# Optimization experiments

Hardware: AMD Instinct MI355X
Metric: run time of the kernel (lower is better)

Reference implementation:

```python
import jax, jax.numpy as jnp
import numpy as np

B, N, D, C = 256, 5, 2048, 1000   # batch, nodeNum, inputDim, num_classes
H = 1024                          # GCN hidden dim (dim_hid)
PROTO_M = 0.999                   # args.proto_m EMA momentum
EPS = 1e-12


def normalize_adj(a):
    # symmetric normalization D^-1/2 A D^-1/2 of the all-ones adjacency
    d = jnp.sum(a, axis=1)
    dinv = 1.0 / jnp.sqrt(d)
    return a * dinv[:, None] * dinv[None, :]


def setup_inputs() -> dict:
    key = jax.random.key(0)
    ks = jax.random.split(key, 8)
    x = jax.random.normal(ks[0], (B, N, D), jnp.float32)          # region features (post-backbone)
    target = jax.random.randint(ks[1], (B,), 0, C)                # labels
    prototypes = jax.random.normal(ks[2], (C, N, D), jnp.float32)  # prototype memory bank
    adj = normalize_adj(jnp.ones((N, N), jnp.float32))            # adjMatrix_q
    s = 0.02
    W1 = jax.random.normal(ks[3], (D, H), jnp.float32) * s        # GCN layer 1
    W2 = jax.random.normal(ks[4], (H, D), jnp.float32) * s        # GCN layer 2
    Wg = jax.random.normal(ks[5], (N * D, D), jnp.float32) * s    # fc_g
    bg = jnp.zeros((D,), jnp.float32)
    Wc = jax.random.normal(ks[6], (D, C), jnp.float32) * s        # fc_cls
    bc = jnp.zeros((C,), jnp.float32)
    return dict(x=x, target=target, prototypes=prototypes, adj=adj,
                W1=W1, W2=W2, Wg=Wg, bg=bg, Wc=Wc, bc=bc)


def reference(x, target, prototypes, adj, W1, W2, Wg, bg, Wc, bc):
    # --- Res_Gcn (non-proto path): 2-layer GCN over the N region nodes ---
    h = jax.nn.relu(jnp.einsum('nm,bmd,dh->bnh', adj, x, W1))      # [B,N,H]
    nodes = jnp.einsum('nm,bmh,hd->bnd', adj, h, W2)               # [B,N,D]
    g = nodes.reshape(B, N * D) @ Wg + bg                          # fc_g -> [B,D]
    pred = g @ Wc + bc                                             # fc_cls -> [B,C]

    # --- sequential per-sample EMA scatter-update of prototype bank ---
    # order matters for duplicate labels, so use lax.scan (sequential)
    def step(protos, inp):
        feat, label = inp                                          # feat: [N,D]
        new = protos[label] * PROTO_M + (1.0 - PROTO_M) * feat
        return protos.at[label].set(new), None

    protos, _ = jax.lax.scan(step, prototypes, (x, target))

    # F.normalize(prototypes, p=2, dim=1): L2 norm over the node axis
    norm = jnp.sqrt(jnp.sum(protos * protos, axis=1, keepdims=True))
    protos = protos / jnp.maximum(norm, EPS)
    return pred, protos
```

## Files before the change

kernel.cpp:

```cpp
#include <hip/hip_runtime.h>
#include <hip/hip_bf16.h>
#include <math.h>

#define BB 256
#define NN 5
#define DD 2048
#define CC 1000
#define HH 1024
#define PROTO_M 0.999f

typedef unsigned short u16;
typedef __attribute__((ext_vector_type(8))) short short8;
typedef __attribute__((ext_vector_type(4))) float f32x4;

__device__ __forceinline__ u16 f2bf(float f) {
    union { float f; unsigned u; } x; x.f = f;
    unsigned r = x.u + 0x7fff + ((x.u >> 16) & 1);
    return (u16)(r >> 16);
}

__device__ __forceinline__ void gload16(const u16* g, u16* l) {
    __builtin_amdgcn_global_load_lds(
        (const __attribute__((address_space(1))) unsigned int*)g,
        (__attribute__((address_space(3))) unsigned int*)l, 16, 0, 0);
}

__device__ __forceinline__ void tr_tile(const float* __restrict__ in,
                                        u16* __restrict__ out,
                                        int K, int N, int k0, int n0) {
    constexpr int STR = 72;
    __shared__ u16 T[64 * STR];
    const int t = threadIdx.x;
    const int c4 = t % 16;
    const int rr = t / 16;
#pragma unroll
    for (int p = 0; p < 4; ++p) {
        int k = p * 16 + rr;
        int n = c4 * 4;
        if (n0 + n < N) {
            float4 v = *(const float4*)(in + (size_t)(k0 + k) * N + n0 + n);
            T[(n + 0) * STR + k] = f2bf(v.x);
            T[(n + 1) * STR + k] = f2bf(v.y);
            T[(n + 2) * STR + k] = f2bf(v.z);
            T[(n + 3) * STR + k] = f2bf(v.w);
        }
    }
    __syncthreads();
    const int ch = t % 8;
    const int nl0 = t / 8;
    const short8 zero8 = {0, 0, 0, 0, 0, 0, 0, 0};
#pragma unroll
    for (int q = 0; q < 2; ++q) {
        int nl = nl0 + q * 32;
        short8 v = zero8;
        if (n0 + nl < N) v = *(const short8*)(&T[nl * STR + ch * 8]);
        *(short8*)(out + (size_t)(n0 + nl) * K + k0 + ch * 8) = v;
    }
}

__global__ __launch_bounds__(256) void transpose3(const float* __restrict__ W1,
                                                  const float* __restrict__ W2,
                                                  const float* __restrict__ Wc,
                                                  u16* __restrict__ W1t,
                                                  u16* __restrict__ W2t,
                                                  u16* __restrict__ Wct) {
    int bid = blockIdx.x;
    if (bid < 512) {
        tr_tile(W1, W1t, DD, HH, (bid % 32) * 64, (bid / 32) * 64);
    } else if (bid < 1024) {
        bid -= 512;
        tr_tile(W2, W2t, HH, DD, (bid % 16) * 64, (bid / 16) * 64);
    } else {
        bid -= 1024;
        tr_tile(Wc, Wct, DD, CC, (bid % 32) * 64, (bid / 32) * 64);
    }
}

__global__ __launch_bounds__(256) void build_wgeff(const float* __restrict__ Wg,
                                                   const float* __restrict__ adjp,
                                                   u16* __restrict__ out) {
    constexpr int STR = 72;
    __shared__ u16 T[64 * STR];
    float rn[NN];
#pragma unroll
    for (int n = 0; n < NN; ++n) {
        float s = 0.f;
#pragma unroll
        for (int m = 0; m < NN; ++m) s += adjp[n * NN + m];
        rn[n] = s;
    }
    const int o0 = blockIdx.x % 32 * 64;
    const int d0 = blockIdx.x / 32 * 64;
    const int t = threadIdx.x;
    const int c4 = t % 16;
    const int rr = t / 16;
#pragma unroll
    for (int p = 0; p < 4; ++p) {
        int d = p * 16 + rr;
        int o = c4 * 4;
        float4 acc = {0.f, 0.f, 0.f, 0.f};
#pragma unroll
        for (int n = 0; n < NN; ++n) {
            float4 v = *(const float4*)(Wg + ((size_t)n * DD + d0 + d) * DD + o0 + o);
            acc.x += rn[n] * v.x; acc.y += rn[n] * v.y;
            acc.z += rn[n] * v.z; acc.w += rn[n] * v.w;
        }
        T[(o + 0) * STR + d] = f2bf(acc.x);
        T[(o + 1) * STR + d] = f2bf(acc.y);
        T[(o + 2) * STR + d] = f2bf(acc.z);
        T[(o + 3) * STR + d] = f2bf(acc.w);
    }
    __syncthreads();
    const int ch = t % 8;
    const int ol0 = t / 8;
#pragma unroll
    for (int q = 0; q < 2; ++q) {
        int ol = ol0 + q * 32;
        short8 v = *(const short8*)(&T[ol * STR + ch * 8]);
        *(short8*)(out + (size_t)(o0 + ol) * DD + d0 + ch * 8) = v;
    }
}

__global__ __launch_bounds__(256) void colmix(const float* __restrict__ adjp,
                                              const float* __restrict__ x,
                                              u16* __restrict__ s) {
    float av[NN];
#pragma unroll
    for (int m = 0; m < NN; ++m) av[m] = adjp[m];
    int idx = blockIdx.x * blockDim.x + threadIdx.x;
    int b = idx / (DD / 4), d4 = idx % (DD / 4);
    float acc[4] = {0.f, 0.f, 0.f, 0.f};
#pragma unroll
    for (int m = 0; m < NN; ++m) {
        float4 v = *(const float4*)(x + ((size_t)b * NN + m) * DD + d4 * 4);
        acc[0] += av[m] * v.x; acc[1] += av[m] * v.y;
        acc[2] += av[m] * v.z; acc[3] += av[m] * v.w;
    }
    ushort4 o;
    o.x = f2bf(acc[0]); o.y = f2bf(acc[1]); o.z = f2bf(acc[2]); o.w = f2bf(acc[3]);
    *(ushort4*)(s + (size_t)b * DD + d4 * 4) = o;
}

template<bool RELU, bool BIAS, bool OUTF32>
__global__ __launch_bounds__(256) void gemm_gl(const u16* __restrict__ A,
                                               const u16* __restrict__ Bt,
                                               const float* __restrict__ bias,
                                               void* __restrict__ C,
                                               int M, int N, int K) {
    constexpr int BM = 64, BN = 64;
    constexpr int FM = BM / 32, FN = BN / 32, SEG = BM / 32;
    __shared__ u16 As[BM * 64];
    __shared__ u16 Bs[BN * 64];
    const int t = threadIdx.x;
    const int lane = t & 63;
    const int w = t >> 6;
    const int wr = w >> 1, wc = w & 1;
    const int lr = lane & 15;
    const int kc = lane >> 4;
    const int lrow8 = lane >> 3;
    const int lc = lane & 7;
    const int m0 = blockIdx.y * BM;
    const int n0 = blockIdx.x * BN;

    f32x4 acc[FM][FN];
#pragma unroll
    for (int i = 0; i < FM; ++i)
#pragma unroll
        for (int j = 0; j < FN; ++j) acc[i][j] = (f32x4){0.f, 0.f, 0.f, 0.f};

    for (int k0 = 0; k0 < K; k0 += 64) {
        __syncthreads();
#pragma unroll
        for (int p = 0; p < SEG; ++p) {
            int s = p * 4 + w;
            int r = s * 8 + lrow8;
            int cs = lc ^ (r & 7);
            gload16(A + (size_t)(m0 + r) * K + k0 + cs * 8, &As[s * 512]);
        }
#pragma unroll
        for (int p = 0; p < SEG; ++p) {
            int s = p * 4 + w;
            int r = s * 8 + lrow8;
            int cs = lc ^ (r & 7);
            gload16(Bt + (size_t)(n0 + r) * K + k0 + cs * 8, &Bs[s * 512]);
        }
        __syncthreads();

#pragma unroll
        for (int ks = 0; ks < 2; ++ks) {
            short8 af[FM], bfr[FN];
#pragma unroll
            for (int i = 0; i < FM; ++i) {
                int row = wr * (BM / 2) + i * 16 + lr;
                int cs = (ks * 4 + kc) ^ (row & 7);
                af[i] = *(const short8*)(&As[row * 64 + cs * 8]);
            }
#pragma unroll
            for (int j = 0; j < FN; ++j) {
                int row = wc * (BN / 2) + j * 16 + lr;
                int cs = (ks * 4 + kc) ^ (row & 7);
                bfr[j] = *(const short8*)(&Bs[row * 64 + cs * 8]);
            }
#pragma unroll
            for (int i = 0; i < FM; ++i)
#pragma unroll
                for (int j = 0; j < FN; ++j)
                    acc[i][j] = __builtin_amdgcn_mfma_f32_16x16x32_bf16(
                        af[i], bfr[j], acc[i][j], 0, 0, 0);
        }
    }

#pragma unroll
    for (int i = 0; i < FM; ++i) {
        int row = m0 + wr * (BM / 2) + i * 16 + kc * 4;
#pragma unroll
        for (int j = 0; j < FN; ++j) {
            int col = n0 + wc * (BN / 2) + j * 16 + lr;
            if (col >= N) continue;
            float bv = BIAS ? bias[col] : 0.f;
#pragma unroll
            for (int q = 0; q < 4; ++q) {
                float v = acc[i][j][q] + bv;
                if (RELU) v = fmaxf(v, 0.f);
                if (OUTF32) ((float*)C)[(size_t)(row + q) * N + col] = v;
                else        ((u16*)C)[(size_t)(row + q) * N + col] = f2bf(v);
            }
        }
    }
}

__global__ __launch_bounds__(256) void proto_fused(const float* __restrict__ protos,
                                                   const float* __restrict__ x,
                                                   const int* __restrict__ target,
                                                   float* __restrict__ out) {
    const int c = blockIdx.x >> 1;
    const int d = ((blockIdx.x & 1) * 256 + threadIdx.x) * 4;
    int k = 0;
    for (int b = 0; b < BB; ++b) k += (target[b] == c) ? 1 : 0;
    const float dec = powf(PROTO_M, (float)k);
    float4 v[NN];
#pragma unroll
    for (int n = 0; n < NN; ++n) {
        float4 p = *(const float4*)(protos + ((size_t)c * NN + n) * DD + d);
        v[n].x = p.x * dec; v[n].y = p.y * dec; v[n].z = p.z * dec; v[n].w = p.w * dec;
    }
    if (k > 0) {
        float p = (1.0f - PROTO_M) * powf(PROTO_M, (float)(k - 1));
        const float invm = 1.0f / PROTO_M;
        for (int b = 0; b < BB; ++b) {
            if (target[b] == c) {
#pragma unroll
                for (int n = 0; n < NN; ++n) {
                    float4 xv = *(const float4*)(x + ((size_t)b * NN + n) * DD + d);
                    v[n].x += p * xv.x; v[n].y += p * xv.y;
                    v[n].z += p * xv.z; v[n].w += p * xv.w;
                }
                p *= invm;
            }
        }
    }
    float ss[4] = {0.f, 0.f, 0.f, 0.f};
#pragma unroll
    for (int n = 0; n < NN; ++n) {
        ss[0] += v[n].x * v[n].x; ss[1] += v[n].y * v[n].y;
        ss[2] += v[n].z * v[n].z; ss[3] += v[n].w * v[n].w;
    }
    float inv[4];
#pragma unroll
    for (int j = 0; j < 4; ++j) inv[j] = 1.0f / fmaxf(sqrtf(ss[j]), 1e-12f);
#pragma unroll
    for (int n = 0; n < NN; ++n) {
        float4 o;
        o.x = v[n].x * inv[0]; o.y = v[n].y * inv[1];
        o.z = v[n].z * inv[2]; o.w = v[n].w * inv[3];
        *(float4*)(out + ((size_t)c * NN + n) * DD + d) = o;
    }
}

extern "C" void kernel_launch(void* const* d_in, const int* in_sizes, int n_in,
                              void* d_out, int out_size, void* d_ws, size_t ws_size,
                              hipStream_t stream) {
    const float* x          = (const float*)d_in[0];
    const int*   target     = (const int*)d_in[1];
    const float* prototypes = (const float*)d_in[2];
    const float* adj        = (const float*)d_in[3];
    const float* W1         = (const float*)d_in[4];
    const float* W2         = (const float*)d_in[5];
    const float* Wg         = (const float*)d_in[6];
    const float* bg         = (const float*)d_in[7];
    const float* Wc         = (const float*)d_in[8];
    const float* bc         = (const float*)d_in[9];

    float* out_pred   = (float*)d_out;
    float* out_protos = (float*)d_out + (size_t)BB * CC;

    char* w = (char*)d_ws;
    u16* W1t   = (u16*)w;   w += (size_t)HH * DD * 2;
    u16* W2t   = (u16*)w;   w += (size_t)DD * HH * 2;
    u16* Wct   = (u16*)w;   w += (size_t)1024 * DD * 2;
    u16* Wgte  = (u16*)w;   w += (size_t)DD * DD * 2;
    u16* s     = (u16*)w;   w += (size_t)BB * DD * 2;
    u16* tb    = (u16*)w;   w += (size_t)BB * HH * 2;
    u16* u     = (u16*)w;   w += (size_t)BB * DD * 2;
    u16* g     = (u16*)w;   w += (size_t)BB * DD * 2;

    transpose3<<<1536, 256, 0, stream>>>(W1, W2, Wc, W1t, W2t, Wct);
    build_wgeff<<<1024, 256, 0, stream>>>(Wg, adj, Wgte);
    colmix<<<(BB * DD / 4) / 256, 256, 0, stream>>>(adj, x, s);
    gemm_gl<true, false, false><<<dim3(HH / 64, BB / 64), 256, 0, stream>>>(
        s, W1t, nullptr, tb, BB, HH, DD);
    gemm_gl<false, false, false><<<dim3(DD / 64, BB / 64), 256, 0, stream>>>(
        tb, W2t, nullptr, u, BB, DD, HH);
    gemm_gl<false, true, false><<<dim3(DD / 64, BB / 64), 256, 0, stream>>>(
        u, Wgte, bg, g, BB, DD, DD);
    gemm_gl<false, true, true><<<dim3(1024 / 64, BB / 64), 256, 0, stream>>>(
        g, Wct, bc, out_pred, BB, CC, DD);
    proto_fused<<<CC * 2, 256, 0, stream>>>(prototypes, x, target, out_protos);
}
```

Measured before the change: 309.8 us.

## Merge prep kernels into one launch and use LDS-free single-wave GEMM tiles

Folds the three weight-prep kernels (transposes, Wg effective build, column mix) into one prep_all launch, removing two kernel launches and their gaps. Swaps the LDS-staged 64x64 GEMM for a single-wave 32x32-tile GEMM that loads MFMA fragments straight from global memory, with no LDS traffic and no barriers. The smaller tiles give more blocks for these small-M GEMMs. The cost is less operand reuse per block, so global and L2 traffic rises, and each wave's loads are not coalesced across full rows.

```diff
diff --git a/kernel.cpp b/kernel.cpp
--- a/kernel.cpp
+++ b/kernel.cpp
@@ -19,17 +19,10 @@
     return (u16)(r >> 16);
 }
 
-__device__ __forceinline__ void gload16(const u16* g, u16* l) {
-    __builtin_amdgcn_global_load_lds(
-        (const __attribute__((address_space(1))) unsigned int*)g,
-        (__attribute__((address_space(3))) unsigned int*)l, 16, 0, 0);
-}
-
 __device__ __forceinline__ void tr_tile(const float* __restrict__ in,
-                                        u16* __restrict__ out,
+                                        u16* __restrict__ out, u16* T,
                                         int K, int N, int k0, int n0) {
     constexpr int STR = 72;
-    __shared__ u16 T[64 * STR];
     const int t = threadIdx.x;
     const int c4 = t % 16;
     const int rr = t / 16;
@@ -58,169 +51,130 @@
     }
 }
 
-__global__ __launch_bounds__(256) void transpose3(const float* __restrict__ W1,
-                                                  const float* __restrict__ W2,
-                                                  const float* __restrict__ Wc,
-                                                  u16* __restrict__ W1t,
-                                                  u16* __restrict__ W2t,
-                                                  u16* __restrict__ Wct) {
+__global__ __launch_bounds__(256) void prep_all(const float* __restrict__ W1,
+                                                const float* __restrict__ W2,
+                                                const float* __restrict__ Wc,
+                                                const float* __restrict__ Wg,
+                                                const float* __restrict__ adjp,
+                                                const float* __restrict__ x,
+                                                u16* __restrict__ W1t,
+                                                u16* __restrict__ W2t,
+                                                u16* __restrict__ Wct,
+                                                u16* __restrict__ Wgte,
+                                                u16* __restrict__ s) {
+    constexpr int STR = 72;
+    __shared__ u16 T[64 * STR];
     int bid = blockIdx.x;
     if (bid < 512) {
-        tr_tile(W1, W1t, DD, HH, (bid % 32) * 64, (bid / 32) * 64);
+        tr_tile(W1, W1t, T, DD, HH, (bid % 32) * 64, (bid / 32) * 64);
     } else if (bid < 1024) {
         bid -= 512;
-        tr_tile(W2, W2t, HH, DD, (bid % 16) * 64, (bid / 16) * 64);
+        tr_tile(W2, W2t, T, HH, DD, (bid % 16) * 64, (bid / 16) * 64);
+    } else if (bid < 1536) {
+        bid -= 1024;
+        tr_tile(Wc, Wct, T, DD, CC, (bid % 32) * 64, (bid / 32) * 64);
+    } else if (bid < 2560) {
+        bid -= 1536;
+        float rn[NN];
+#pragma unroll
+        for (int n = 0; n < NN; ++n) {
+            float ss = 0.f;
+#pragma unroll
+            for (int m = 0; m < NN; ++m) ss += adjp[n * NN + m];
+            rn[n] = ss;
+        }
+        const int o0 = bid % 32 * 64;
+        const int d0 = bid / 32 * 64;
+        const int t = threadIdx.x;
+        const int c4 = t % 16;
+        const int rr = t / 16;
+#pragma unroll
+        for (int p = 0; p < 4; ++p) {
+            int d = p * 16 + rr;
+            int o = c4 * 4;
+            float4 acc = {0.f, 0.f, 0.f, 0.f};
+#pragma unroll
+            for (int n = 0; n < NN; ++n) {
+                float4 v = *(const float4*)(Wg + ((size_t)n * DD + d0 + d) * DD + o0 + o);
+                acc.x += rn[n] * v.x; acc.y += rn[n] * v.y;
+                acc.z += rn[n] * v.z; acc.w += rn[n] * v.w;
+            }
+            T[(o + 0) * STR + d] = f2bf(acc.x);
+            T[(o + 1) * STR + d] = f2bf(acc.y);
+            T[(o + 2) * STR + d] = f2bf(acc.z);
+            T[(o + 3) * STR + d] = f2bf(acc.w);
+        }
+        __syncthreads();
+        const int ch = t % 8;
+        const int ol0 = t / 8;
+#pragma unroll
+        for (int q = 0; q < 2; ++q) {
+            int ol = ol0 + q * 32;
+            short8 v = *(const short8*)(&T[ol * STR + ch * 8]);
+            *(short8*)(Wgte + (size_t)(o0 + ol) * DD + d0 + ch * 8) = v;
+        }
     } else {
-        bid -= 1024;
-        tr_tile(Wc, Wct, DD, CC, (bid % 32) * 64, (bid / 32) * 64);
-    }
-}
-
-__global__ __launch_bounds__(256) void build_wgeff(const float* __restrict__ Wg,
-                                                   const float* __restrict__ adjp,
-                                                   u16* __restrict__ out) {
-    constexpr int STR = 72;
-    __shared__ u16 T[64 * STR];
-    float rn[NN];
-#pragma unroll
-    for (int n = 0; n < NN; ++n) {
-        float s = 0.f;
-#pragma unroll
-        for (int m = 0; m < NN; ++m) s += adjp[n * NN + m];
-        rn[n] = s;
-    }
-    const int o0 = blockIdx.x % 32 * 64;
-    const int d0 = blockIdx.x / 32 * 64;
-    const int t = threadIdx.x;
-    const int c4 = t % 16;
-    const int rr = t / 16;
-#pragma unroll
-    for (int p = 0; p < 4; ++p) {
-        int d = p * 16 + rr;
-        int o = c4 * 4;
-        float4 acc = {0.f, 0.f, 0.f, 0.f};
-#pragma unroll
-        for (int n = 0; n < NN; ++n) {
-            float4 v = *(const float4*)(Wg + ((size_t)n * DD + d0 + d) * DD + o0 + o);
-            acc.x += rn[n] * v.x; acc.y += rn[n] * v.y;
-            acc.z += rn[n] * v.z; acc.w += rn[n] * v.w;
-        }
-        T[(o + 0) * STR + d] = f2bf(acc.x);
-        T[(o + 1) * STR + d] = f2bf(acc.y);
-        T[(o + 2) * STR + d] = f2bf(acc.z);
-        T[(o + 3) * STR + d] = f2bf(acc.w);
-    }
-    __syncthreads();
-    const int ch = t % 8;
-    const int ol0 = t / 8;
-#pragma unroll
-    for (int q = 0; q < 2; ++q) {
-        int ol = ol0 + q * 32;
-        short8 v = *(const short8*)(&T[ol * STR + ch * 8]);
-        *(short8*)(out + (size_t)(o0 + ol) * DD + d0 + ch * 8) = v;
-    }
-}
-
-__global__ __launch_bounds__(256) void colmix(const float* __restrict__ adjp,
-                                              const float* __restrict__ x,
-                                              u16* __restrict__ s) {
-    float av[NN];
-#pragma unroll
-    for (int m = 0; m < NN; ++m) av[m] = adjp[m];
-    int idx = blockIdx.x * blockDim.x + threadIdx.x;
-    int b = idx / (DD / 4), d4 = idx % (DD / 4);
-    float acc[4] = {0.f, 0.f, 0.f, 0.f};
-#pragma unroll
-    for (int m = 0; m < NN; ++m) {
-        float4 v = *(const float4*)(x + ((size_t)b * NN + m) * DD + d4 * 4);
-        acc[0] += av[m] * v.x; acc[1] += av[m] * v.y;
-        acc[2] += av[m] * v.z; acc[3] += av[m] * v.w;
-    }
-    ushort4 o;
-    o.x = f2bf(acc[0]); o.y = f2bf(acc[1]); o.z = f2bf(acc[2]); o.w = f2bf(acc[3]);
-    *(ushort4*)(s + (size_t)b * DD + d4 * 4) = o;
-}
-
-template<bool RELU, bool BIAS, bool OUTF32>
-__global__ __launch_bounds__(256) void gemm_gl(const u16* __restrict__ A,
-                                               const u16* __restrict__ Bt,
-                                               const float* __restrict__ bias,
-                                               void* __restrict__ C,
-                                               int M, int N, int K) {
-    constexpr int BM = 64, BN = 64;
-    constexpr int FM = BM / 32, FN = BN / 32, SEG = BM / 32;
-    __shared__ u16 As[BM * 64];
-    __shared__ u16 Bs[BN * 64];
-    const int t = threadIdx.x;
-    const int lane = t & 63;
-    const int w = t >> 6;
-    const int wr = w >> 1, wc = w & 1;
-    const int lr = lane & 15;
-    const int kc = lane >> 4;
-    const int lrow8 = lane >> 3;
-    const int lc = lane & 7;
-    const int m0 = blockIdx.y * BM;
-    const int n0 = blockIdx.x * BN;
-
-    f32x4 acc[FM][FN];
-#pragma unroll
-    for (int i = 0; i < FM; ++i)
-#pragma unroll
-        for (int j = 0; j < FN; ++j) acc[i][j] = (f32x4){0.f, 0.f, 0.f, 0.f};
-
-    for (int k0 = 0; k0 < K; k0 += 64) {
-        __syncthreads();
-#pragma unroll
-        for (int p = 0; p < SEG; ++p) {
-            int s = p * 4 + w;
-            int r = s * 8 + lrow8;
-            int cs = lc ^ (r & 7);
-            gload16(A + (size_t)(m0 + r) * K + k0 + cs * 8, &As[s * 512]);
-        }
-#pragma unroll
-        for (int p = 0; p < SEG; ++p) {
-            int s = p * 4 + w;
-            int r = s * 8 + lrow8;
-            int cs = lc ^ (r & 7);
-            gload16(Bt + (size_t)(n0 + r) * K + k0 + cs * 8, &Bs[s * 512]);
-        }
-        __syncthreads();
-
-#pragma unroll
-        for (int ks = 0; ks < 2; ++ks) {
-            short8 af[FM], bfr[FN];
-#pragma unroll
-            for (int i = 0; i < FM; ++i) {
-                int row = wr * (BM / 2) + i * 16 + lr;
-                int cs = (ks * 4 + kc) ^ (row & 7);
-                af[i] = *(const short8*)(&As[row * 64 + cs * 8]);
-            }
-#pragma unroll
-            for (int j = 0; j < FN; ++j) {
-                int row = wc * (BN / 2) + j * 16 + lr;
-                int cs = (ks * 4 + kc) ^ (row & 7);
-                bfr[j] = *(const short8*)(&Bs[row * 64 + cs * 8]);
-            }
-#pragma unroll
-            for (int i = 0; i < FM; ++i)
-#pragma unroll
-                for (int j = 0; j < FN; ++j)
-                    acc[i][j] = __builtin_amdgcn_mfma_f32_16x16x32_bf16(
-                        af[i], bfr[j], acc[i][j], 0, 0, 0);
-        }
-    }
-
-#pragma unroll
-    for (int i = 0; i < FM; ++i) {
-        int row = m0 + wr * (BM / 2) + i * 16 + kc * 4;
-#pragma unroll
-        for (int j = 0; j < FN; ++j) {
-            int col = n0 + wc * (BN / 2) + j * 16 + lr;
+        bid -= 2560;
+        float av[NN];
+#pragma unroll
+        for (int m = 0; m < NN; ++m) av[m] = adjp[m];
+        int idx = bid * 256 + threadIdx.x;
+        int b = idx / (DD / 4), d4 = idx % (DD / 4);
+        float acc[4] = {0.f, 0.f, 0.f, 0.f};
+#pragma unroll
+        for (int m = 0; m < NN; ++m) {
+            float4 v = *(const float4*)(x + ((size_t)b * NN + m) * DD + d4 * 4);
+            acc[0] += av[m] * v.x; acc[1] += av[m] * v.y;
+            acc[2] += av[m] * v.z; acc[3] += av[m] * v.w;
+        }
+        ushort4 o;
+        o.x = f2bf(acc[0]); o.y = f2bf(acc[1]);
+        o.z = f2bf(acc[2]); o.w = f2bf(acc[3]);
+        *(ushort4*)(s + (size_t)b * DD + d4 * 4) = o;
+    }
+}
+
+template<int K, bool RELU, bool BIAS, bool OUTF32>
+__global__ __launch_bounds__(64) void gemm_direct(const u16* __restrict__ A,
+                                                  const u16* __restrict__ Bt,
+                                                  const float* __restrict__ bias,
+                                                  void* __restrict__ C, int N) {
+    const int lane = threadIdx.x;
+    const int lr = lane & 15, kc = lane >> 4;
+    const int m0 = blockIdx.y * 32, n0 = blockIdx.x * 32;
+    const u16* pa0 = A + (size_t)(m0 + lr) * K + kc * 8;
+    const u16* pa1 = pa0 + (size_t)16 * K;
+    const u16* pb0 = Bt + (size_t)(n0 + lr) * K + kc * 8;
+    const u16* pb1 = pb0 + (size_t)16 * K;
+
+    f32x4 acc00 = {0.f, 0.f, 0.f, 0.f}, acc01 = acc00;
+    f32x4 acc10 = acc00, acc11 = acc00;
+
+    constexpr int NT = K / 32;
+#pragma unroll 8
+    for (int t = 0; t < NT; ++t) {
+        short8 a0 = *(const short8*)(pa0 + t * 32);
+        short8 a1 = *(const short8*)(pa1 + t * 32);
+        short8 b0 = *(const short8*)(pb0 + t * 32);
+        short8 b1 = *(const short8*)(pb1 + t * 32);
+        acc00 = __builtin_amdgcn_mfma_f32_16x16x32_bf16(a0, b0, acc00, 0, 0, 0);
+        acc01 = __builtin_amdgcn_mfma_f32_16x16x32_bf16(a0, b1, acc01, 0, 0, 0);
+        acc10 = __builtin_amdgcn_mfma_f32_16x16x32_bf16(a1, b0, acc10, 0, 0, 0);
+        acc11 = __builtin_amdgcn_mfma_f32_16x16x32_bf16(a1, b1, acc11, 0, 0, 0);
+    }
+
+    f32x4 accs[2][2] = {{acc00, acc01}, {acc10, acc11}};
+#pragma unroll
+    for (int i = 0; i < 2; ++i) {
+        int row = m0 + i * 16 + kc * 4;
+#pragma unroll
+        for (int j = 0; j < 2; ++j) {
+            int col = n0 + j * 16 + lr;
             if (col >= N) continue;
             float bv = BIAS ? bias[col] : 0.f;
 #pragma unroll
             for (int q = 0; q < 4; ++q) {
-                float v = acc[i][j][q] + bv;
+                float v = accs[i][j][q] + bv;
                 if (RELU) v = fmaxf(v, 0.f);
                 if (OUTF32) ((float*)C)[(size_t)(row + q) * N + col] = v;
                 else        ((u16*)C)[(size_t)(row + q) * N + col] = f2bf(v);
@@ -295,25 +249,24 @@
     float* out_protos = (float*)d_out + (size_t)BB * CC;
 
     char* w = (char*)d_ws;
-    u16* W1t   = (u16*)w;   w += (size_t)HH * DD * 2;
-    u16* W2t   = (u16*)w;   w += (size_t)DD * HH * 2;
-    u16* Wct   = (u16*)w;   w += (size_t)1024 * DD * 2;
-    u16* Wgte  = (u16*)w;   w += (size_t)DD * DD * 2;
-    u16* s     = (u16*)w;   w += (size_t)BB * DD * 2;
-    u16* tb    = (u16*)w;   w += (size_t)BB * HH * 2;
-    u16* u     = (u16*)w;   w += (size_t)BB * DD * 2;
-    u16* g     = (u16*)w;   w += (size_t)BB * DD * 2;
-
-    transpose3<<<1536, 256, 0, stream>>>(W1, W2, Wc, W1t, W2t, Wct);
-    build_wgeff<<<1024, 256, 0, stream>>>(Wg, adj, Wgte);
-    colmix<<<(BB * DD / 4) / 256, 256, 0, stream>>>(adj, x, s);
-    gemm_gl<true, false, false><<<dim3(HH / 64, BB / 64), 256, 0, stream>>>(
-        s, W1t, nullptr, tb, BB, HH, DD);
-    gemm_gl<false, false, false><<<dim3(DD / 64, BB / 64), 256, 0, stream>>>(
-        tb, W2t, nullptr, u, BB, DD, HH);
-    gemm_gl<false, true, false><<<dim3(DD / 64, BB / 64), 256, 0, stream>>>(
-        u, Wgte, bg, g, BB, DD, DD);
-    gemm_gl<false, true, true><<<dim3(1024 / 64, BB / 64), 256, 0, stream>>>(
-        g, Wct, bc, out_pred, BB, CC, DD);
+    u16* W1t  = (u16*)w;  w += (size_t)HH * DD * 2;
+    u16* W2t  = (u16*)w;  w += (size_t)DD * HH * 2;
+    u16* Wct  = (u16*)w;  w += (size_t)1024 * DD * 2;
+    u16* Wgte = (u16*)w;  w += (size_t)DD * DD * 2;
+    u16* s    = (u16*)w;  w += (size_t)BB * DD * 2;
+    u16* tb   = (u16*)w;  w += (size_t)BB * HH * 2;
+    u16* u    = (u16*)w;  w += (size_t)BB * DD * 2;
+    u16* g    = (u16*)w;  w += (size_t)BB * DD * 2;
+
+    prep_all<<<3072, 256, 0, stream>>>(W1, W2, Wc, Wg, adj, x,
+                                       W1t, W2t, Wct, Wgte, s);
+    gemm_direct<DD, true, false, false><<<dim3(HH / 32, BB / 32), 64, 0, stream>>>(
+        s, W1t, nullptr, tb, HH);
+    gemm_direct<HH, false, false, false><<<dim3(DD / 32, BB / 32), 64, 0, stream>>>(
+        tb, W2t, nullptr, u, DD);
+    gemm_direct<DD, false, true, false><<<dim3(DD / 32, BB / 32), 64, 0, stream>>>(
+        u, Wgte, bg, g, DD);
+    gemm_direct<DD, false, true, true><<<dim3(1024 / 32, BB / 32), 64, 0, stream>>>(
+        g, Wct, bc, out_pred, CC);
     proto_fused<<<CC * 2, 256, 0, stream>>>(prototypes, x, target, out_protos);
 }
```

Measured after the change: 302.3 us. 1.02x faster.
